# Kernel optimization log

Hardware: AMD Instinct MI355X
Metric: run time of the kernel (lower is better)

Reference implementation:

```python
import jax, jax.numpy as jnp
import numpy as np

N = 50000          # nodes
M_UND = 500000     # undirected edges -> E = 2*M_UND directed messages
Q = 16             # num_groups
MAX_ITER = 10
BP_MAX_DIFF = 0.01


def setup_inputs() -> dict:
    key = jax.random.key(0)
    k1, k2, k3, k4 = jax.random.split(key, 4)
    u = jax.random.randint(k1, (M_UND,), 0, N)
    v = jax.random.randint(k2, (M_UND,), 0, N)
    # each undirected edge (u,v) yields directed messages u->v and v->u
    src = jnp.concatenate([u, v]).astype(jnp.int32)
    dst = jnp.concatenate([v, u]).astype(jnp.int32)
    rev = jnp.concatenate([jnp.arange(M_UND) + M_UND, jnp.arange(M_UND)]).astype(jnp.int32)
    psi0 = jax.random.uniform(k3, (N, Q), dtype=jnp.float32)
    psi0 = psi0 / psi0.sum(1, keepdims=True)
    msg0 = jax.random.uniform(k4, (2 * M_UND, Q), dtype=jnp.float32)
    msg0 = msg0 / msg0.sum(1, keepdims=True)
    c = 2.0 * M_UND / N  # mean degree
    beta = jnp.float32(np.log(Q / np.sqrt(c - 1.0) + 1.0))  # beta_ast init
    return dict(src=src, dst=dst, rev=rev, psi0=psi0, msg0=msg0, beta=beta, n_nodes=N)


def _bp_forward(src, dst, rev, psi0, msg0, beta, n_nodes):
    q = psi0.shape[1]
    n_edges = msg0.shape[0]
    mean_w = float(n_edges) / (float(n_nodes) * float(n_nodes))  # W.mean() for 0/1 weights
    expb_m1 = jnp.exp(beta) - 1.0
    h0 = (-beta * mean_w * psi0).sum(0)  # external field, shape [q]

    def step(carry, _):
        msg, psi, h, done = carry
        # S_e = 1 + psi_{src->dst} * (e^{beta*w} - 1), w == 1
        logS = jnp.log1p(msg * expb_m1)                                    # [E, q]
        node_log = jax.ops.segment_sum(logS, dst, num_segments=n_nodes)    # prod over incoming, log-domain
        # cavity update: message i->j uses all incoming to i except j->i (rev edge)
        new_msg = jax.nn.softmax(node_log[src] - logS[rev] + h, axis=-1)   # exp(h)*prod, normalized
        diff = jnp.max(jnp.abs(jax.lax.stop_gradient(new_msg) -
                               jax.lax.stop_gradient(msg)).sum(-1))
        logS2 = jnp.log1p(new_msg * expb_m1)
        node_log2 = jax.ops.segment_sum(logS2, dst, num_segments=n_nodes)
        new_psi = jax.nn.softmax(node_log2 + h, axis=-1)                    # marginals
        new_h = (-beta * mean_w * new_psi).sum(0)
        # freeze state once converged (mirrors early-return on max_diff < bp_max_diff)
        msg = jnp.where(done, msg, new_msg)
        psi = jnp.where(done, psi, new_psi)
        h = jnp.where(done, h, new_h)
        done = done | (diff < BP_MAX_DIFF)
        return (msg, psi, h, done), diff

    (msg, psi, h, done), _ = jax.lax.scan(
        step, (msg0, psi0, h0, jnp.array(False)), None, length=MAX_ITER)

    # soft modularity: (1/2m) sum_e psi_i . psi_j - sum_g (sum_i d_i psi_ig / 2m)^2
    m2 = float(n_edges)  # total directed edge weight (= 2m for unit weights)
    deg = jax.ops.segment_sum(jnp.ones((n_edges,), psi.dtype), dst, num_segments=n_nodes)
    edge_term = jnp.einsum('eq,eq->', psi[src], psi[dst]) / m2
    deg_term = jnp.sum((jnp.einsum('n,nq->q', deg, psi) / m2) ** 2)
    modularity = edge_term - deg_term
    # group-balance regularizer, scaled by sqrt(q) as in forward()
    reg = jnp.sum((psi.sum(0) / float(n_nodes) - 1.0 / q) ** 2) * np.sqrt(q)
    # mean per-node entropy of marginals, normalized by log(q)
    entropy_loss = jnp.mean(-jnp.sum(psi * jnp.log(psi + 1e-12), axis=-1)) / np.log(q)
    return psi, reg, entropy_loss, modularity


def reference(src, dst, rev, psi0, msg0, beta, n_nodes):
    return _bp_forward(src, dst, rev, psi0, msg0, beta, n_nodes)
```

## Files before the change

### kernel.cpp

```cpp
#include <hip/hip_runtime.h>

#define Q 16
#define SCAN_B 256

__device__ __forceinline__ float wsum(float v){
  #pragma unroll
  for(int o=32;o;o>>=1) v += __shfl_xor(v,o);
  return v;
}
__device__ __forceinline__ float wmaxr(float v){
  #pragma unroll
  for(int o=32;o;o>>=1) v = fmaxf(v,__shfl_xor(v,o));
  return v;
}

__global__ void __launch_bounds__(256, 8) k_edgeF(
    const int* __restrict__ src, const int* __restrict__ dst,
    const int* __restrict__ ipos,
    const float* __restrict__ msgIn, float* __restrict__ msgA,
    float* __restrict__ msgB, const float* __restrict__ nl,
    const float* __restrict__ betap,
    const float* __restrict__ hsrc, int nch,
    const float* __restrict__ diffprev, int nbd,
    float* __restrict__ diffout, float* __restrict__ hout,
    int* __restrict__ donep, int M, float mean_w, int k)
{
  if (*donep) return;
  const float beta = *betap;
  const float eb = __expf(beta) - 1.0f;
  const int t = threadIdx.x;
  __shared__ float smf[16][17];
  __shared__ float hq_sm[16];
  __shared__ float smx[4];
  __shared__ int brk;
  {
    const int g = t>>4, qq = t&15;
    float s = 0.0f;
    for (int r = g; r < nch; r += 16) s += hsrc[(size_t)r*Q + qq];
    smf[g][qq] = s; __syncthreads();
    if (t < Q){
      float tot = 0.0f;
      #pragma unroll
      for (int i=0;i<16;i++) tot += smf[i][t];
      hq_sm[t] = -beta * mean_w * tot;
    }
  }
  if (k > 0){
    float dm = 0.0f;
    for (int i = t; i < nbd; i += 256) dm = fmaxf(dm, diffprev[i]);
    dm = wmaxr(dm);
    if ((t & 63) == 0) smx[t>>6] = dm;
    __syncthreads();
    if (t == 0)
      brk = (fmaxf(fmaxf(smx[0],smx[1]), fmaxf(smx[2],smx[3])) < 0.01f);
    __syncthreads();
    if (brk){ if (blockIdx.x == 0 && t == 0) *donep = 1; return; }
  } else {
    __syncthreads();
  }
  if (blockIdx.x == 0 && t < Q) hout[t] = hq_sm[t];
  const float hq = hq_sm[t & 15];

  const int q = t & 15;
  const int grp  = (blockIdx.x*blockDim.x + t) >> 4;
  const int ngrp = (gridDim.x*blockDim.x) >> 4;
  float dloc = 0.0f;
  for (int p = grp; p < M; p += ngrp){
    const int u = src[p], v = dst[p];
    const int i0 = ipos[p], i1 = ipos[p + M];
    const float m0 = msgIn[(size_t)p*Q + q];
    const float m1 = msgIn[((size_t)p + (size_t)M)*Q + q];
    const float nu = nl[(size_t)u*Q + q];
    const float nv = nl[(size_t)v*Q + q];
    float t0 = nu - __logf(fmaf(m1, eb, 1.0f)) + hq;
    float t1 = nv - __logf(fmaf(m0, eb, 1.0f)) + hq;
    float x0=t0, x1=t1;
    #pragma unroll
    for (int o=1;o<16;o<<=1){
      x0=fmaxf(x0,__shfl_xor(x0,o)); x1=fmaxf(x1,__shfl_xor(x1,o));
    }
    const float e0=__expf(t0-x0), e1=__expf(t1-x1);
    float s0=e0, s1=e1;
    #pragma unroll
    for (int o=1;o<16;o<<=1){ s0+=__shfl_xor(s0,o); s1+=__shfl_xor(s1,o); }
    const float n0=e0/s0, n1=e1/s1;
    float d0=fabsf(n0-m0), d1=fabsf(n1-m1);
    #pragma unroll
    for (int o=1;o<16;o<<=1){ d0+=__shfl_xor(d0,o); d1+=__shfl_xor(d1,o); }
    dloc = fmaxf(dloc, fmaxf(d0,d1));
    msgA[(size_t)p*Q + q] = n0;
    msgA[((size_t)p + (size_t)M)*Q + q] = n1;
    msgB[(size_t)i0*Q + q] = n0;
    msgB[(size_t)i1*Q + q] = n1;
  }
  float wm = wmaxr(dloc);
  if ((t & 63) == 0) smx[t>>6] = wm;
  __syncthreads();
  if (t == 0)
    diffout[blockIdx.x] = fmaxf(fmaxf(smx[0],smx[1]), fmaxf(smx[2],smx[3]));
}

__global__ void __launch_bounds__(256, 8) k_gatherF2(
    const float* __restrict__ msgB, const int* __restrict__ offs,
    float* __restrict__ nl, const float* __restrict__ hk,
    float* __restrict__ psi, const float* __restrict__ betap,
    const int* __restrict__ donep, float* __restrict__ hp2k,
    int N, int mode)
{
  if (mode && *donep) return;
  const int wid = threadIdx.x >> 6;
  const int n = blockIdx.x*4 + wid;
  const float eb = __expf(*betap) - 1.0f;
  const int lane = threadIdx.x & 63;
  const int sub = lane >> 4, q16 = lane & 15;
  int start = 0, end = 0;
  if (n < N){ start = offs[n]; end = offs[n+1]; }
  float acc = 0.0f;
  int i = start + sub;
  for (; i + 4 < end; i += 8){
    const float x0 = msgB[(size_t)i*Q + q16];
    const float x1 = msgB[(size_t)(i+4)*Q + q16];
    acc += __logf(fmaf(x0, eb, 1.0f)) + __logf(fmaf(x1, eb, 1.0f));
  }
  if (i < end) acc += __logf(fmaf(msgB[(size_t)i*Q + q16], eb, 1.0f));
  acc += __shfl_xor(acc, 16);
  acc += __shfl_xor(acc, 32);
  if (n < N && sub == 0) nl[(size_t)n*Q + q16] = acc;
  if (!mode) return;
  float t = acc + hk[q16];
  float m = t;
  #pragma unroll
  for (int o=1;o<16;o<<=1) m = fmaxf(m, __shfl_xor(m,o));
  float ex = __expf(t-m);
  float s = ex;
  #pragma unroll
  for (int o=1;o<16;o<<=1) s += __shfl_xor(s,o);
  const float pq = ex/s;
  if (n < N && sub == 0) psi[(size_t)n*Q + q16] = pq;
  __shared__ float smh[4][17];
  if (sub == 0) smh[wid][q16] = (n < N) ? pq : 0.0f;
  __syncthreads();
  if (threadIdx.x < Q)
    unsafeAtomicAdd(&hp2k[(size_t)(blockIdx.x>>6)*Q + threadIdx.x],
      smh[0][threadIdx.x]+smh[1][threadIdx.x]+smh[2][threadIdx.x]+smh[3][threadIdx.x]);
}

__global__ void __launch_bounds__(256, 8) k_h_part(
    const float* __restrict__ psi, float* __restrict__ hpart, int N)
{
  const int n = blockIdx.x*blockDim.x + threadIdx.x;
  float pv[Q];
  if (n < N) {
    const float4* a = (const float4*)(psi + (size_t)n*Q);
    #pragma unroll
    for (int i=0;i<4;i++){ float4 t=a[i]; pv[4*i]=t.x; pv[4*i+1]=t.y; pv[4*i+2]=t.z; pv[4*i+3]=t.w; }
  } else {
    #pragma unroll
    for (int q=0;q<Q;q++) pv[q]=0.0f;
  }
  __shared__ float sm[4][Q];
  const int wid = threadIdx.x>>6, lane = threadIdx.x&63;
  #pragma unroll
  for (int q=0;q<Q;q++){
    float s = wsum(pv[q]);
    if (lane == 0) sm[wid][q] = s;
  }
  __syncthreads();
  if (threadIdx.x < Q)
    hpart[(size_t)blockIdx.x*Q + threadIdx.x] =
      sm[0][threadIdx.x]+sm[1][threadIdx.x]+sm[2][threadIdx.x]+sm[3][threadIdx.x];
}

__global__ void __launch_bounds__(256, 8) k_deg(
    const int* __restrict__ dst, int* __restrict__ deg, int E)
{
  const int e = blockIdx.x*blockDim.x + threadIdx.x;
  if (e < E) atomicAdd(&deg[dst[e]], 1);
}

__global__ void __launch_bounds__(SCAN_B) k_scan1(
    const int* __restrict__ deg, int* __restrict__ offs,
    int* __restrict__ bsum, int N)
{
  __shared__ int sm[SCAN_B];
  const int i = blockIdx.x*SCAN_B + threadIdx.x;
  const int v = (i<N) ? deg[i] : 0;
  sm[threadIdx.x] = v; __syncthreads();
  #pragma unroll
  for (int o=1;o<SCAN_B;o<<=1){
    int t = (threadIdx.x>=o) ? sm[threadIdx.x-o] : 0;
    __syncthreads();
    sm[threadIdx.x] += t;
    __syncthreads();
  }
  if (i<N) offs[i] = sm[threadIdx.x] - v;
  if (threadIdx.x==SCAN_B-1) bsum[blockIdx.x] = sm[threadIdx.x];
}

__global__ void __launch_bounds__(SCAN_B) k_scan2(int* __restrict__ bsum, int nb)
{
  __shared__ int sm[SCAN_B];
  const int v = (threadIdx.x<nb) ? bsum[threadIdx.x] : 0;
  sm[threadIdx.x] = v; __syncthreads();
  #pragma unroll
  for (int o=1;o<SCAN_B;o<<=1){
    int t = (threadIdx.x>=o) ? sm[threadIdx.x-o] : 0;
    __syncthreads();
    sm[threadIdx.x] += t;
    __syncthreads();
  }
  if (threadIdx.x<nb) bsum[threadIdx.x] = sm[threadIdx.x] - v;
}

__global__ void __launch_bounds__(SCAN_B) k_scan3(
    int* __restrict__ offs, int* __restrict__ cursor,
    const int* __restrict__ bsum, int N, int E)
{
  const int i = blockIdx.x*SCAN_B + threadIdx.x;
  if (i<N){
    const int o = offs[i] + bsum[blockIdx.x];
    offs[i] = o; cursor[i] = o;
  }
  if (i==0) offs[N] = E;
}

__global__ void __launch_bounds__(256, 8) k_fillCS(
    const int* __restrict__ dst, int* __restrict__ cursor,
    const float* __restrict__ msg0, float* __restrict__ msgB,
    int* __restrict__ ipos, int E)
{
  const int e = blockIdx.x*blockDim.x + threadIdx.x;
  if (e >= E) return;
  const int ip = atomicAdd(&cursor[dst[e]], 1);
  ipos[e] = ip;
  const float4* s = (const float4*)(msg0 + (size_t)e*Q);
  float4* d = (float4*)(msgB + (size_t)ip*Q);
  float4 x0=s[0], x1=s[1], x2=s[2], x3=s[3];
  d[0]=x0; d[1]=x1; d[2]=x2; d[3]=x3;
}

__global__ void __launch_bounds__(256, 8) k_stats(
    const int* __restrict__ src, const int* __restrict__ dst,
    const float* __restrict__ psi, const int* __restrict__ deg,
    float* __restrict__ colpart, float* __restrict__ degpart,
    float* __restrict__ entpart, float* __restrict__ edgepart,
    int* __restrict__ cnt, float* __restrict__ out,
    int M, int N, int NQ, float m2, int gS)
{
  const int t = threadIdx.x;
  const int lane = t & 63, wid = t >> 6;
  float ed = 0.0f;
  for (int p = blockIdx.x*256 + t; p < M; p += gS*256){
    const int u = src[p], v = dst[p];
    const float4* a = (const float4*)(psi + (size_t)u*Q);
    const float4* b = (const float4*)(psi + (size_t)v*Q);
    float d = 0.0f;
    #pragma unroll
    for (int i=0;i<4;i++){
      float4 x=a[i], y=b[i];
      d += x.x*y.x + x.y*y.y + x.z*y.z + x.w*y.w;
    }
    ed += 2.0f*d;
  }
  float ca[Q], da[Q]; float ea = 0.0f;
  #pragma unroll
  for (int q=0;q<Q;q++){ ca[q]=0.0f; da[q]=0.0f; }
  for (int n = blockIdx.x*256 + t; n < N; n += gS*256){
    const float4* a = (const float4*)(psi + (size_t)n*Q);
    float pv[Q];
    #pragma unroll
    for (int i=0;i<4;i++){ float4 x=a[i]; pv[4*i]=x.x; pv[4*i+1]=x.y; pv[4*i+2]=x.z; pv[4*i+3]=x.w; }
    const float dg = (float)deg[n];
    #pragma unroll
    for (int q=0;q<Q;q++){
      ca[q] += pv[q];
      da[q] += pv[q]*dg;
      ea    -= pv[q]*__logf(pv[q]+1e-12f);
    }
  }
  __shared__ float smc[4][17], smd[4][17];
  __shared__ float sme[4], smeE[4];
  __shared__ float smg[16][17], smg2[16][17];
  __shared__ int amL;
  #pragma unroll
  for (int q=0;q<Q;q++){
    float s  = wsum(ca[q]);
    float s2 = wsum(da[q]);
    if (lane == 0){ smc[wid][q]=s; smd[wid][q]=s2; }
  }
  float se = wsum(ea);
  float sed = wsum(ed);
  if (lane == 0){ sme[wid]=se; smeE[wid]=sed; }
  __syncthreads();
  if (t < Q){
    colpart[(size_t)blockIdx.x*Q+t] = smc[0][t]+smc[1][t]+smc[2][t]+smc[3][t];
    degpart[(size_t)blockIdx.x*Q+t] = smd[0][t]+smd[1][t]+smd[2][t]+smd[3][t];
  }
  if (t == 0){
    entpart[blockIdx.x]  = sme[0]+sme[1]+sme[2]+sme[3];
    edgepart[blockIdx.x] = smeE[0]+smeE[1]+smeE[2]+smeE[3];
  }
  __threadfence();
  if (t == 0) amL = (atomicAdd(cnt, 1) == gS-1);
  __syncthreads();
  if (!amL) return;
  {
    const int g = t>>4, qq = t&15;
    float cs=0.0f, ds=0.0f;
    for (int r = g; r < gS; r += 16){
      cs += colpart[(size_t)r*Q + qq];
      ds += degpart[(size_t)r*Q + qq];
    }
    smg[g][qq] = cs; smg2[g][qq] = ds;
    __syncthreads();
    float colq=0.0f, degq=0.0f;
    if (t < Q){
      #pragma unroll
      for (int i=0;i<16;i++){ colq += smg[i][t]; degq += smg2[i][t]; }
    }
    float es=0.0f, en=0.0f;
    for (int i=t; i<gS; i+=256){ es += edgepart[i]; en += entpart[i]; }
    es = wsum(es); en = wsum(en);
    if (lane == 0){ smeE[wid]=es; sme[wid]=en; }
    __syncthreads();
    if (t < Q){ smg[0][t] = colq; smg2[0][t] = degq; }
    __syncthreads();
    if (t == 0){
      const float edge_total = smeE[0]+smeE[1]+smeE[2]+smeE[3];
      const float ent_total  = sme[0]+sme[1]+sme[2]+sme[3];
      float reg = 0.0f, dt = 0.0f;
      for (int i=0;i<Q;i++){
        float d = smg[0][i]/(float)N - 1.0f/(float)Q; reg += d*d;
        float s = smg2[0][i]/m2; dt += s*s;
      }
      out[NQ+0] = reg * 4.0f;
      out[NQ+1] = ent_total/(float)N / 2.7725887222397811f;
      out[NQ+2] = edge_total/m2 - dt;
    }
  }
}

extern "C" void kernel_launch(void* const* d_in, const int* in_sizes, int n_in,
                              void* d_out, int out_size, void* d_ws, size_t ws_size,
                              hipStream_t stream)
{
  const int*   src   = (const int*)  d_in[0];
  const int*   dst   = (const int*)  d_in[1];
  const float* psi0  = (const float*)d_in[3];
  const float* msg0  = (const float*)d_in[4];
  const float* betap = (const float*)d_in[5];

  const int E  = in_sizes[0];
  const int M  = E/2;
  const int NQ = in_sizes[3];
  const int N  = NQ/Q;
  const float mean_w = (float)((double)E/((double)N*(double)N));
  const float m2 = (float)E;

  const int B = 256;
  const int gE = (E+B-1)/B, gN = (N+B-1)/B;
  const int nb = (N+SCAN_B-1)/SCAN_B;
  const int nbE = 2048;
  const int gW = (N+3)/4;
  const int nchG = (gW+63)>>6;
  const int gS = 256;

  char* w = (char*)d_ws;
  float* msgA    = (float*)w; w += (size_t)E*Q*sizeof(float);
  float* msgB    = (float*)w; w += (size_t)E*Q*sizeof(float);
  float* nl      = (float*)w; w += (size_t)NQ*sizeof(float);
  int*   ipos    = (int*)  w; w += (size_t)E*sizeof(int);
  int*   offs    = (int*)  w; w += (size_t)(N+16)*sizeof(int);
  int*   cursor  = (int*)  w; w += (size_t)(N+16)*sizeof(int);
  int*   bsum    = (int*)  w; w += 256*sizeof(int);
  float* hp0     = (float*)w; w += (size_t)gN*Q*sizeof(float);
  float* edgepart= (float*)w; w += (size_t)gS*sizeof(float);
  float* colpart = (float*)w; w += (size_t)gS*Q*sizeof(float);
  float* degpart = (float*)w; w += (size_t)gS*Q*sizeof(float);
  float* entpart = (float*)w; w += (size_t)gS*sizeof(float);
  int*   deg     = (int*)  w; w += (size_t)(N+16)*sizeof(int);
  float* hpart2  = (float*)w; w += (size_t)10*nchG*Q*sizeof(float);
  float* diffpart= (float*)w; w += (size_t)10*nbE*sizeof(float);
  float* harr    = (float*)w; w += (size_t)10*Q*sizeof(float);
  int*   donep   = (int*)  w; w += 4*sizeof(int);
  int*   cnts    = (int*)  w; w += 4*sizeof(int);

  float* psi = (float*)d_out;

  const size_t small_bytes = (size_t)((char*)w - (char*)deg);
  hipMemsetAsync(deg, 0, small_bytes, stream);

  k_h_part  <<<gN,B,0,stream>>>(psi0, hp0, N);
  k_deg     <<<gE,B,0,stream>>>(dst, deg, E);
  k_scan1   <<<nb,SCAN_B,0,stream>>>(deg, offs, bsum, N);
  k_scan2   <<<1, SCAN_B,0,stream>>>(bsum, nb);
  k_scan3   <<<nb,SCAN_B,0,stream>>>(offs, cursor, bsum, N, E);
  k_fillCS  <<<gE,B,0,stream>>>(dst, cursor, msg0, msgB, ipos, E);
  k_gatherF2<<<gW,B,0,stream>>>(msgB, offs, nl, harr, psi, betap, donep,
                                hpart2, N, 0);

  for (int k=0; k<10; ++k) {
    const float* mi  = (k==0) ? msg0 : msgA;
    const float* hs  = (k==0) ? hp0 : (hpart2 + (size_t)(k-1)*nchG*Q);
    const int    nch = (k==0) ? gN : nchG;
    const float* dp  = diffpart + (size_t)(k>0 ? k-1 : 0)*nbE;
    k_edgeF   <<<nbE,B,0,stream>>>(src, dst, ipos, mi, msgA, msgB, nl, betap,
                                   hs, nch, dp, nbE,
                                   diffpart + (size_t)k*nbE, harr + (size_t)k*Q,
                                   donep, M, mean_w, k);
    k_gatherF2<<<gW,B,0,stream>>>(msgB, offs, nl, harr + (size_t)k*Q, psi,
                                  betap, donep,
                                  hpart2 + (size_t)k*nchG*Q, N, 1);
  }

  k_stats<<<gS,B,0,stream>>>(src, dst, psi, deg, colpart, degpart,
                             entpart, edgepart, cnts, psi, M, N, NQ, m2, gS);
}
```

Measured before the change: 967.9 us.

## Fuse BP iteration loop into a single persistent cooperative kernel with grid syncs

Replaces the 21 separate edge-update and gather kernel launches with one persistent cooperative kernel sized to full occupancy. Iterations are separated by grid-wide barriers, and the convergence check becomes a uniform break, replacing the done flag. The goal is to remove per-launch overhead and launch gaps across the ten iterations. In exchange, the grid is capped at resident blocks, so each thread loops over more work, and each grid.sync adds its own barrier cost.

```diff
diff --git a/kernel.cpp b/kernel.cpp
--- a/kernel.cpp
+++ b/kernel.cpp
@@ -1,4 +1,7 @@
 #include <hip/hip_runtime.h>
+#include <hip/hip_cooperative_groups.h>
+
+namespace cg = cooperative_groups;
 
 #define Q 16
 #define SCAN_B 256
@@ -14,135 +17,161 @@
   return v;
 }
 
-__global__ void __launch_bounds__(256, 8) k_edgeF(
+__global__ void __launch_bounds__(256, 8) k_bploop(
     const int* __restrict__ src, const int* __restrict__ dst,
-    const int* __restrict__ ipos,
-    const float* __restrict__ msgIn, float* __restrict__ msgA,
-    float* __restrict__ msgB, const float* __restrict__ nl,
-    const float* __restrict__ betap,
-    const float* __restrict__ hsrc, int nch,
-    const float* __restrict__ diffprev, int nbd,
-    float* __restrict__ diffout, float* __restrict__ hout,
-    int* __restrict__ donep, int M, float mean_w, int k)
-{
-  if (*donep) return;
+    const int* __restrict__ ipos, const int* __restrict__ offs,
+    const float* __restrict__ msg0, float* __restrict__ msgA,
+    float* __restrict__ msgB, float* __restrict__ nl,
+    const float* __restrict__ hp0, int nh0,
+    float* __restrict__ hpart2, int nch,
+    float* __restrict__ diffpart,
+    const float* __restrict__ betap, float* __restrict__ psi,
+    int M, int N, float mean_w)
+{
+  cg::grid_group grid = cg::this_grid();
+  const int nb  = gridDim.x;
+  const int bid = blockIdx.x;
+  const int t   = threadIdx.x;
+  const int lane = t & 63;
+  const int sub  = lane >> 4, q16 = lane & 15;
   const float beta = *betap;
-  const float eb = __expf(beta) - 1.0f;
-  const int t = threadIdx.x;
+  const float eb   = __expf(beta) - 1.0f;
+  const int gw  = (bid*256 + t) >> 6;
+  const int nwv = (nb*256) >> 6;
+  const int grp = (bid*256 + t) >> 4;
+  const int ngrp = (nb*256) >> 4;
+
   __shared__ float smf[16][17];
   __shared__ float hq_sm[16];
   __shared__ float smx[4];
+  __shared__ float smh[4][17];
   __shared__ int brk;
-  {
-    const int g = t>>4, qq = t&15;
-    float s = 0.0f;
-    for (int r = g; r < nch; r += 16) s += hsrc[(size_t)r*Q + qq];
-    smf[g][qq] = s; __syncthreads();
-    if (t < Q){
-      float tot = 0.0f;
-      #pragma unroll
-      for (int i=0;i<16;i++) tot += smf[i][t];
-      hq_sm[t] = -beta * mean_w * tot;
-    }
-  }
-  if (k > 0){
-    float dm = 0.0f;
-    for (int i = t; i < nbd; i += 256) dm = fmaxf(dm, diffprev[i]);
-    dm = wmaxr(dm);
-    if ((t & 63) == 0) smx[t>>6] = dm;
-    __syncthreads();
-    if (t == 0)
-      brk = (fmaxf(fmaxf(smx[0],smx[1]), fmaxf(smx[2],smx[3])) < 0.01f);
-    __syncthreads();
-    if (brk){ if (blockIdx.x == 0 && t == 0) *donep = 1; return; }
-  } else {
-    __syncthreads();
-  }
-  if (blockIdx.x == 0 && t < Q) hout[t] = hq_sm[t];
-  const float hq = hq_sm[t & 15];
-
-  const int q = t & 15;
-  const int grp  = (blockIdx.x*blockDim.x + t) >> 4;
-  const int ngrp = (gridDim.x*blockDim.x) >> 4;
-  float dloc = 0.0f;
-  for (int p = grp; p < M; p += ngrp){
-    const int u = src[p], v = dst[p];
-    const int i0 = ipos[p], i1 = ipos[p + M];
-    const float m0 = msgIn[(size_t)p*Q + q];
-    const float m1 = msgIn[((size_t)p + (size_t)M)*Q + q];
-    const float nu = nl[(size_t)u*Q + q];
-    const float nv = nl[(size_t)v*Q + q];
-    float t0 = nu - __logf(fmaf(m1, eb, 1.0f)) + hq;
-    float t1 = nv - __logf(fmaf(m0, eb, 1.0f)) + hq;
-    float x0=t0, x1=t1;
-    #pragma unroll
-    for (int o=1;o<16;o<<=1){
-      x0=fmaxf(x0,__shfl_xor(x0,o)); x1=fmaxf(x1,__shfl_xor(x1,o));
-    }
-    const float e0=__expf(t0-x0), e1=__expf(t1-x1);
-    float s0=e0, s1=e1;
-    #pragma unroll
-    for (int o=1;o<16;o<<=1){ s0+=__shfl_xor(s0,o); s1+=__shfl_xor(s1,o); }
-    const float n0=e0/s0, n1=e1/s1;
-    float d0=fabsf(n0-m0), d1=fabsf(n1-m1);
-    #pragma unroll
-    for (int o=1;o<16;o<<=1){ d0+=__shfl_xor(d0,o); d1+=__shfl_xor(d1,o); }
-    dloc = fmaxf(dloc, fmaxf(d0,d1));
-    msgA[(size_t)p*Q + q] = n0;
-    msgA[((size_t)p + (size_t)M)*Q + q] = n1;
-    msgB[(size_t)i0*Q + q] = n0;
-    msgB[(size_t)i1*Q + q] = n1;
-  }
-  float wm = wmaxr(dloc);
-  if ((t & 63) == 0) smx[t>>6] = wm;
-  __syncthreads();
-  if (t == 0)
-    diffout[blockIdx.x] = fmaxf(fmaxf(smx[0],smx[1]), fmaxf(smx[2],smx[3]));
-}
-
-__global__ void __launch_bounds__(256, 8) k_gatherF2(
-    const float* __restrict__ msgB, const int* __restrict__ offs,
-    float* __restrict__ nl, const float* __restrict__ hk,
-    float* __restrict__ psi, const float* __restrict__ betap,
-    const int* __restrict__ donep, float* __restrict__ hp2k,
-    int N, int mode)
-{
-  if (mode && *donep) return;
-  const int wid = threadIdx.x >> 6;
-  const int n = blockIdx.x*4 + wid;
-  const float eb = __expf(*betap) - 1.0f;
-  const int lane = threadIdx.x & 63;
-  const int sub = lane >> 4, q16 = lane & 15;
-  int start = 0, end = 0;
-  if (n < N){ start = offs[n]; end = offs[n+1]; }
-  float acc = 0.0f;
-  int i = start + sub;
-  for (; i + 4 < end; i += 8){
-    const float x0 = msgB[(size_t)i*Q + q16];
-    const float x1 = msgB[(size_t)(i+4)*Q + q16];
-    acc += __logf(fmaf(x0, eb, 1.0f)) + __logf(fmaf(x1, eb, 1.0f));
-  }
-  if (i < end) acc += __logf(fmaf(msgB[(size_t)i*Q + q16], eb, 1.0f));
-  acc += __shfl_xor(acc, 16);
-  acc += __shfl_xor(acc, 32);
-  if (n < N && sub == 0) nl[(size_t)n*Q + q16] = acc;
-  if (!mode) return;
-  float t = acc + hk[q16];
-  float m = t;
-  #pragma unroll
-  for (int o=1;o<16;o<<=1) m = fmaxf(m, __shfl_xor(m,o));
-  float ex = __expf(t-m);
-  float s = ex;
-  #pragma unroll
-  for (int o=1;o<16;o<<=1) s += __shfl_xor(s,o);
-  const float pq = ex/s;
-  if (n < N && sub == 0) psi[(size_t)n*Q + q16] = pq;
-  __shared__ float smh[4][17];
-  if (sub == 0) smh[wid][q16] = (n < N) ? pq : 0.0f;
-  __syncthreads();
-  if (threadIdx.x < Q)
-    unsafeAtomicAdd(&hp2k[(size_t)(blockIdx.x>>6)*Q + threadIdx.x],
-      smh[0][threadIdx.x]+smh[1][threadIdx.x]+smh[2][threadIdx.x]+smh[3][threadIdx.x]);
+
+  for (int n = gw; n < N; n += nwv){
+    const int s0 = offs[n], e0 = offs[n+1];
+    float acc = 0.0f;
+    int i = s0 + sub;
+    for (; i + 4 < e0; i += 8){
+      const float x0 = msgB[(size_t)i*Q + q16];
+      const float x1 = msgB[(size_t)(i+4)*Q + q16];
+      acc += __logf(fmaf(x0, eb, 1.0f)) + __logf(fmaf(x1, eb, 1.0f));
+    }
+    if (i < e0) acc += __logf(fmaf(msgB[(size_t)i*Q + q16], eb, 1.0f));
+    acc += __shfl_xor(acc, 16);
+    acc += __shfl_xor(acc, 32);
+    if (sub == 0) nl[(size_t)n*Q + q16] = acc;
+  }
+  grid.sync();
+
+  for (int k = 0; k < 10; ++k){
+    {
+      const float* hsrc = (k==0) ? hp0 : (hpart2 + (size_t)(k-1)*nch*Q);
+      const int nrows   = (k==0) ? nh0 : nch;
+      const int g = t>>4, qq = t&15;
+      float s = 0.0f;
+      for (int r = g; r < nrows; r += 16) s += hsrc[(size_t)r*Q + qq];
+      smf[g][qq] = s; __syncthreads();
+      if (t < Q){
+        float tot = 0.0f;
+        #pragma unroll
+        for (int i=0;i<16;i++) tot += smf[i][t];
+        hq_sm[t] = -beta * mean_w * tot;
+      }
+    }
+    if (k > 0){
+      const float* dp = diffpart + (size_t)(k-1)*nb;
+      float dm = 0.0f;
+      for (int i = t; i < nb; i += 256) dm = fmaxf(dm, dp[i]);
+      dm = wmaxr(dm);
+      if (lane == 0) smx[t>>6] = dm;
+      __syncthreads();
+      if (t == 0)
+        brk = (fmaxf(fmaxf(smx[0],smx[1]), fmaxf(smx[2],smx[3])) < 0.01f);
+      __syncthreads();
+      if (brk) break;
+    } else {
+      __syncthreads();
+    }
+    const float hq = hq_sm[q16];
+
+    const float* msgIn = (k==0) ? msg0 : msgA;
+    float dloc = 0.0f;
+    for (int p = grp; p < M; p += ngrp){
+      const int u = src[p], v = dst[p];
+      const int i0 = ipos[p], i1 = ipos[p + M];
+      const float m0 = msgIn[(size_t)p*Q + q16];
+      const float m1 = msgIn[((size_t)p + (size_t)M)*Q + q16];
+      const float nu = nl[(size_t)u*Q + q16];
+      const float nv = nl[(size_t)v*Q + q16];
+      float t0 = nu - __logf(fmaf(m1, eb, 1.0f)) + hq;
+      float t1 = nv - __logf(fmaf(m0, eb, 1.0f)) + hq;
+      float x0=t0, x1=t1;
+      #pragma unroll
+      for (int o=1;o<16;o<<=1){
+        x0=fmaxf(x0,__shfl_xor(x0,o)); x1=fmaxf(x1,__shfl_xor(x1,o));
+      }
+      const float e0=__expf(t0-x0), e1=__expf(t1-x1);
+      float s0=e0, s1=e1;
+      #pragma unroll
+      for (int o=1;o<16;o<<=1){ s0+=__shfl_xor(s0,o); s1+=__shfl_xor(s1,o); }
+      const float n0=e0/s0, n1=e1/s1;
+      float d0=fabsf(n0-m0), d1=fabsf(n1-m1);
+      #pragma unroll
+      for (int o=1;o<16;o<<=1){ d0+=__shfl_xor(d0,o); d1+=__shfl_xor(d1,o); }
+      dloc = fmaxf(dloc, fmaxf(d0,d1));
+      msgA[(size_t)p*Q + q16] = n0;
+      msgA[((size_t)p + (size_t)M)*Q + q16] = n1;
+      msgB[(size_t)i0*Q + q16] = n0;
+      msgB[(size_t)i1*Q + q16] = n1;
+    }
+    {
+      float wm = wmaxr(dloc);
+      if (lane == 0) smx[t>>6] = wm;
+      __syncthreads();
+      if (t == 0)
+        diffpart[(size_t)k*nb + bid] =
+          fmaxf(fmaxf(smx[0],smx[1]), fmaxf(smx[2],smx[3]));
+    }
+    grid.sync();
+
+    float* hp2k = hpart2 + (size_t)k*nch*Q;
+    float hacc = 0.0f;
+    for (int n = gw; n < N; n += nwv){
+      const int s0 = offs[n], e0 = offs[n+1];
+      float acc = 0.0f;
+      int i = s0 + sub;
+      for (; i + 4 < e0; i += 8){
+        const float x0 = msgB[(size_t)i*Q + q16];
+        const float x1 = msgB[(size_t)(i+4)*Q + q16];
+        acc += __logf(fmaf(x0, eb, 1.0f)) + __logf(fmaf(x1, eb, 1.0f));
+      }
+      if (i < e0) acc += __logf(fmaf(msgB[(size_t)i*Q + q16], eb, 1.0f));
+      acc += __shfl_xor(acc, 16);
+      acc += __shfl_xor(acc, 32);
+      if (sub == 0) nl[(size_t)n*Q + q16] = acc;
+      float tv = acc + hq_sm[q16];
+      float m = tv;
+      #pragma unroll
+      for (int o=1;o<16;o<<=1) m = fmaxf(m, __shfl_xor(m,o));
+      float ex = __expf(tv-m);
+      float ss = ex;
+      #pragma unroll
+      for (int o=1;o<16;o<<=1) ss += __shfl_xor(ss,o);
+      const float pq = ex/ss;
+      if (sub == 0){
+        psi[(size_t)n*Q + q16] = pq;
+        hacc += pq;
+      }
+    }
+    __syncthreads();
+    if (sub == 0) smh[t>>6][q16] = hacc;
+    else if (lane < 16) ;
+    __syncthreads();
+    if (t < Q)
+      unsafeAtomicAdd(&hp2k[(size_t)(bid>>6)*Q + t],
+        smh[0][t]+smh[1][t]+smh[2][t]+smh[3][t]);
+    grid.sync();
+  }
 }
 
 __global__ void __launch_bounds__(256, 8) k_h_part(
@@ -360,10 +389,18 @@
   const int B = 256;
   const int gE = (E+B-1)/B, gN = (N+B-1)/B;
   const int nb = (N+SCAN_B-1)/SCAN_B;
-  const int nbE = 2048;
-  const int gW = (N+3)/4;
-  const int nchG = (gW+63)>>6;
   const int gS = 256;
+
+  int dev = 0; hipGetDevice(&dev);
+  int nCU = 256;
+  hipDeviceGetAttribute(&nCU, hipDeviceAttributeMultiprocessorCount, dev);
+  int bpc = 1;
+  hipOccupancyMaxActiveBlocksPerMultiprocessor(&bpc, (const void*)k_bploop, 256, 0);
+  if (bpc < 1) bpc = 1;
+  int nbC = nCU * bpc;
+  if (nbC > 2048) nbC = 2048;
+  const int NBMAX = 2048;
+  const int nch = (nbC + 63) >> 6;
 
   char* w = (char*)d_ws;
   float* msgA    = (float*)w; w += (size_t)E*Q*sizeof(float);
@@ -379,10 +416,8 @@
   float* degpart = (float*)w; w += (size_t)gS*Q*sizeof(float);
   float* entpart = (float*)w; w += (size_t)gS*sizeof(float);
   int*   deg     = (int*)  w; w += (size_t)(N+16)*sizeof(int);
-  float* hpart2  = (float*)w; w += (size_t)10*nchG*Q*sizeof(float);
-  float* diffpart= (float*)w; w += (size_t)10*nbE*sizeof(float);
-  float* harr    = (float*)w; w += (size_t)10*Q*sizeof(float);
-  int*   donep   = (int*)  w; w += 4*sizeof(int);
+  float* hpart2  = (float*)w; w += (size_t)10*64*Q*sizeof(float);
+  float* diffpart= (float*)w; w += (size_t)10*NBMAX*sizeof(float);
   int*   cnts    = (int*)  w; w += 4*sizeof(int);
 
   float* psi = (float*)d_out;
@@ -390,28 +425,22 @@
   const size_t small_bytes = (size_t)((char*)w - (char*)deg);
   hipMemsetAsync(deg, 0, small_bytes, stream);
 
-  k_h_part  <<<gN,B,0,stream>>>(psi0, hp0, N);
-  k_deg     <<<gE,B,0,stream>>>(dst, deg, E);
-  k_scan1   <<<nb,SCAN_B,0,stream>>>(deg, offs, bsum, N);
-  k_scan2   <<<1, SCAN_B,0,stream>>>(bsum, nb);
-  k_scan3   <<<nb,SCAN_B,0,stream>>>(offs, cursor, bsum, N, E);
-  k_fillCS  <<<gE,B,0,stream>>>(dst, cursor, msg0, msgB, ipos, E);
-  k_gatherF2<<<gW,B,0,stream>>>(msgB, offs, nl, harr, psi, betap, donep,
-                                hpart2, N, 0);
-
-  for (int k=0; k<10; ++k) {
-    const float* mi  = (k==0) ? msg0 : msgA;
-    const float* hs  = (k==0) ? hp0 : (hpart2 + (size_t)(k-1)*nchG*Q);
-    const int    nch = (k==0) ? gN : nchG;
-    const float* dp  = diffpart + (size_t)(k>0 ? k-1 : 0)*nbE;
-    k_edgeF   <<<nbE,B,0,stream>>>(src, dst, ipos, mi, msgA, msgB, nl, betap,
-                                   hs, nch, dp, nbE,
-                                   diffpart + (size_t)k*nbE, harr + (size_t)k*Q,
-                                   donep, M, mean_w, k);
-    k_gatherF2<<<gW,B,0,stream>>>(msgB, offs, nl, harr + (size_t)k*Q, psi,
-                                  betap, donep,
-                                  hpart2 + (size_t)k*nchG*Q, N, 1);
-  }
+  k_h_part<<<gN,B,0,stream>>>(psi0, hp0, N);
+  k_deg   <<<gE,B,0,stream>>>(dst, deg, E);
+  k_scan1 <<<nb,SCAN_B,0,stream>>>(deg, offs, bsum, N);
+  k_scan2 <<<1, SCAN_B,0,stream>>>(bsum, nb);
+  k_scan3 <<<nb,SCAN_B,0,stream>>>(offs, cursor, bsum, N, E);
+  k_fillCS<<<gE,B,0,stream>>>(dst, cursor, msg0, msgB, ipos, E);
+
+  int Mi=M, Ni=N, nh0=gN, nchi=nch; float mwi=mean_w;
+  void* args[] = {
+    (void*)&src, (void*)&dst, (void*)&ipos, (void*)&offs,
+    (void*)&msg0, (void*)&msgA, (void*)&msgB, (void*)&nl,
+    (void*)&hp0, (void*)&nh0, (void*)&hpart2, (void*)&nchi,
+    (void*)&diffpart, (void*)&betap, (void*)&psi,
+    (void*)&Mi, (void*)&Ni, (void*)&mwi
+  };
+  hipLaunchCooperativeKernel((void*)k_bploop, dim3(nbC), dim3(256), args, 0, stream);
 
   k_stats<<<gS,B,0,stream>>>(src, dst, psi, deg, colpart, degpart,
                              entpart, edgepart, cnts, psi, M, N, NQ, m2, gS);
```

Measured after the change: 3.490 ms. 261% more time.
